# Optimization experiments

Measured on AMD Instinct MI355X. Metric: run time of the kernel, lower is better.

The kernel has to match this reference:

```python
import jax, jax.numpy as jnp
import numpy as np

B, N, C, KV = 4, 4096, 1024, 1024
H = 4            # hardcoded 4-way split in the source
Ch, Kh = C // H, KV // H
EPS = 1e-5       # InstanceNorm2d default eps


def setup_inputs() -> dict:
    key = jax.random.key(0)
    ks = jax.random.split(key, 12)
    s = 0.02
    return {
        "emb1":     jax.random.normal(ks[0], (B, N, C),  jnp.float32),
        "emb_all":  jax.random.normal(ks[1], (B, N, KV), jnp.float32),
        "embd1":    jax.random.normal(ks[2], (B, N, C),  jnp.float32),
        "emb_alld": jax.random.normal(ks[3], (B, N, KV), jnp.float32),
        # per-head query weights (distinct per split), torch Linear layout [out,in]
        "Wq":   jax.random.normal(ks[4],  (H, Ch, Ch), jnp.float32) * s,
        "Wqd":  jax.random.normal(ks[5],  (H, Ch, Ch), jnp.float32) * s,
        # source reuses key[0]/value[0] for all splits -> single shared weight
        "Wk0":  jax.random.normal(ks[6],  (Kh, Kh), jnp.float32) * s,
        "Wv0":  jax.random.normal(ks[7],  (Kh, Kh), jnp.float32) * s,
        "Wkd0": jax.random.normal(ks[8],  (Kh, Kh), jnp.float32) * s,
        "Wvd0": jax.random.normal(ks[9],  (Kh, Kh), jnp.float32) * s,
        "Wout":  jax.random.normal(ks[10], (C, C), jnp.float32) * s,
        "Woutd": jax.random.normal(ks[11], (C, C), jnp.float32) * s,
    }


def _inorm(s):
    # InstanceNorm2d(affine=False): normalize over the (C/4, KV/4) plane per (b, head)
    m = s.mean(axis=(2, 3), keepdims=True)
    v = ((s - m) ** 2).mean(axis=(2, 3), keepdims=True)
    return (s - m) * jax.lax.rsqrt(v + EPS)


def reference(emb1, emb_all, embd1, emb_alld,
              Wq, Wqd, Wk0, Wv0, Wkd0, Wvd0, Wout, Woutd):
    scale = 1.0 / np.sqrt(KV).astype(np.float32)
    # split into 4 channel groups and project (Q: per-group weight; K/V: shared weight)
    Q  = jnp.einsum('bnhc,hoc->bhno', emb1.reshape(B, N, H, Ch),  Wq)    # [B,H,N,Ch]
    Qd = jnp.einsum('bnhc,hoc->bhno', embd1.reshape(B, N, H, Ch), Wqd)
    K  = jnp.einsum('bnhk,ok->bhno', emb_all.reshape(B, N, H, Kh),  Wk0)  # [B,H,N,Kh]
    V  = jnp.einsum('bnhk,ok->bhno', emb_all.reshape(B, N, H, Kh),  Wv0)
    Kd = jnp.einsum('bnhk,ok->bhno', emb_alld.reshape(B, N, H, Kh), Wkd0)
    Vd = jnp.einsum('bnhk,ok->bhno', emb_alld.reshape(B, N, H, Kh), Wvd0)
    # channel-attention scores: contract over tokens N -> [B,H,Ch,Kh]
    s1  = jnp.einsum('bhnc,bhnk->bhck', Q,  Kd) * scale
    sd1 = jnp.einsum('bhnc,bhnk->bhck', Qd, K)  * scale
    p1  = jax.nn.softmax(_inorm(s1),  axis=-1)
    pd1 = jax.nn.softmax(_inorm(sd1), axis=-1)
    # context: probs @ V^T -> [b,h,c,n]; permute(0,3,2,1)+view -> [B,N,C] (c-major, h-minor)
    ctx1  = jnp.einsum('bhck,bhnk->bnch', p1,  Vd).reshape(B, N, C)
    ctxd1 = jnp.einsum('bhck,bhnk->bnch', pd1, V ).reshape(B, N, C)
    O1  = ctx1  @ Wout.T
    Od1 = ctxd1 @ Woutd.T
    return (O1, Od1)
```

## Files before the change

kernel.cpp:

```cpp
#include <hip/hip_runtime.h>
#include <math.h>


#define PITCH 40

typedef __bf16 bf16x4 __attribute__((ext_vector_type(4)));
typedef __bf16 bf16x8 __attribute__((ext_vector_type(8)));
typedef float f32x4 __attribute__((ext_vector_type(4)));

__device__ inline void gl2lds16(const void* g, void* l) {
    __builtin_amdgcn_global_load_lds(
        (const __attribute__((address_space(1))) unsigned int*)g,
        (__attribute__((address_space(3))) unsigned int*)l, 16, 0, 0);
}

__global__ __launch_bounds__(256) void prep_x(const float* __restrict__ emb_all,
                                              const float* __restrict__ emb_alld,
                                              __bf16* __restrict__ Xb) {
    const float* src = blockIdx.y ? emb_alld : emb_all;
    __bf16* dst = Xb + (long long)blockIdx.y * 16777216;
    long long i4 = (long long)blockIdx.x * 256 + threadIdx.x;
    float4 v = *(const float4*)&src[i4 * 4];
    bf16x4 o = {(__bf16)v.x, (__bf16)v.y, (__bf16)v.z, (__bf16)v.w};
    *(bf16x4*)&dst[i4 * 4] = o;
}

__global__ __launch_bounds__(256) void prep_w(
    const float* __restrict__ Wq, const float* __restrict__ Wqd,
    const float* __restrict__ Wk0, const float* __restrict__ Wv0,
    const float* __restrict__ Wkd0, const float* __restrict__ Wvd0,
    const float* __restrict__ Wout, const float* __restrict__ Woutd,
    __bf16* __restrict__ Wq_bf, __bf16* __restrict__ Wk_bf,
    __bf16* __restrict__ WvT_bf, __bf16* __restrict__ WoutR_bf)
{
    int id = blockIdx.x * 256 + threadIdx.x;
    if (id < 524288) {
        Wq_bf[id] = (__bf16)(id < 262144 ? Wq[id] : Wqd[id - 262144]);
    } else if (id < 655360) {
        int j = id - 524288;
        Wk_bf[j] = (__bf16)(j < 65536 ? Wkd0[j] : Wk0[j - 65536]);
    } else if (id < 786432) {
        int j = id - 655360;
        int p = j >> 16, r = (j >> 8) & 255, c2 = j & 255;
        const float* s = p ? Wv0 : Wvd0;
        WvT_bf[j] = (__bf16)s[c2 * 256 + r];
    } else if (id < 2883584) {
        int j = id - 786432;
        int p = j >> 20; int rem = j & 1048575; int h = rem >> 18; int oc = rem & 262143;
        int o = oc >> 8, c = oc & 255;
        const float* s = p ? Woutd : Wout;
        WoutR_bf[j] = (__bf16)s[o * 1024 + c * 4 + h];
    }
}

__global__ __launch_bounds__(256, 2) void gram_mfma(
    const float* __restrict__ emb1, const float* __restrict__ emb_all,
    const float* __restrict__ embd1, const float* __restrict__ emb_alld,
    float* __restrict__ Gpart)
{
    __shared__ __bf16 As[2][128 * PITCH];
    __shared__ __bf16 Bs[2][128 * PITCH];

    const int z = blockIdx.z;
    const int path = z >> 4, bh = z & 15;
    const int b = bh >> 2, h = bh & 3;
    const float* Xm = (path == 0 ? emb_alld : emb_all) + (long long)b * 4194304 + h * 256;
    const float* Xn = (path == 0 ? emb1     : embd1)   + (long long)b * 4194304 + h * 256;

    const int i0 = (blockIdx.x >> 1) * 128;
    const int j0 = (blockIdx.x & 1) * 128;
    const int kb0 = blockIdx.y * 1024;

    const int t = threadIdx.x;
    const int q  = t & 7;
    const int i4 = t >> 3;
    const int lane = t & 63;
    const int wave = t >> 6;
    const int wr = (wave >> 1) * 64, wc = (wave & 1) * 64;
    const int fm = lane & 15, fg = lane >> 4;

    f32x4 acc[4][4];
#pragma unroll
    for (int u = 0; u < 4; ++u)
#pragma unroll
        for (int v = 0; v < 4; ++v) acc[u][v] = (f32x4){0.f, 0.f, 0.f, 0.f};

    const float* pa = Xm + (long long)(kb0 + q * 4) * 1024 + i0 + i4 * 4;
    const float* pb = Xn + (long long)(kb0 + q * 4) * 1024 + j0 + i4 * 4;

    float4 vaA[4], vbA[4], vaB[4], vbB[4];
#pragma unroll
    for (int r = 0; r < 4; ++r) {
        vaA[r] = *(const float4*)(pa + (long long)r * 1024);
        vbA[r] = *(const float4*)(pb + (long long)r * 1024);
    }

#define GRAM_STEP(CURA, CURB, NXTA, NXTB, BUF, SOFF, GUARD)                         \
    do {                                                                            \
        if (GUARD) {                                                                \
            const float* qa = pa + (long long)(SOFF) * 32768;                       \
            const float* qb = pb + (long long)(SOFF) * 32768;                       \
            _Pragma("unroll")                                                       \
            for (int r = 0; r < 4; ++r) {                                           \
                NXTA[r] = *(const float4*)(qa + (long long)r * 1024);               \
                NXTB[r] = *(const float4*)(qb + (long long)r * 1024);               \
            }                                                                       \
        }                                                                           \
        _Pragma("unroll")                                                           \
        for (int cc = 0; cc < 4; ++cc) {                                            \
            bf16x4 wa, wb;                                                          \
            _Pragma("unroll")                                                       \
            for (int r = 0; r < 4; ++r) {                                           \
                wa[r] = (__bf16)(((const float*)&CURA[r])[cc]);                     \
                wb[r] = (__bf16)(((const float*)&CURB[r])[cc]);                     \
            }                                                                       \
            *(bf16x4*)&As[BUF][(i4 * 4 + cc) * PITCH + q * 4] = wa;                 \
            *(bf16x4*)&Bs[BUF][(i4 * 4 + cc) * PITCH + q * 4] = wb;                 \
        }                                                                           \
        asm volatile("s_waitcnt lgkmcnt(0)\ns_barrier" ::: "memory");               \
        bf16x8 af[4], bfv[4];                                                       \
        _Pragma("unroll")                                                           \
        for (int mt = 0; mt < 4; ++mt)                                              \
            af[mt] = *(const bf16x8*)&As[BUF][(wr + mt * 16 + fm) * PITCH + fg * 8];\
        _Pragma("unroll")                                                           \
        for (int nt = 0; nt < 4; ++nt)                                              \
            bfv[nt] = *(const bf16x8*)&Bs[BUF][(wc + nt * 16 + fm) * PITCH + fg * 8];\
        _Pragma("unroll")                                                           \
        for (int mt = 0; mt < 4; ++mt)                                              \
            _Pragma("unroll")                                                       \
            for (int nt = 0; nt < 4; ++nt)                                          \
                acc[mt][nt] = __builtin_amdgcn_mfma_f32_16x16x32_bf16(              \
                    af[mt], bfv[nt], acc[mt][nt], 0, 0, 0);                         \
    } while (0)

    for (int s = 0; s < 32; s += 2) {
        GRAM_STEP(vaA, vbA, vaB, vbB, 0, s + 1, true);
        GRAM_STEP(vaB, vbB, vaA, vbA, 1, s + 2, (s < 30));
    }
#undef GRAM_STEP

    float* Gp = Gpart + ((long long)blockIdx.y * 32 + z) * 65536;
    const int col = lane & 15, rq = (lane >> 4) * 4;
#pragma unroll
    for (int mt = 0; mt < 4; ++mt)
#pragma unroll
        for (int nt = 0; nt < 4; ++nt)
#pragma unroll
            for (int r = 0; r < 4; ++r)
                Gp[(i0 + wr + mt * 16 + rq + r) * 256 + (j0 + wc + nt * 16 + col)] = acc[mt][nt][r];
}

__global__ __launch_bounds__(256) void reduce_g(const float* __restrict__ Gpart, __bf16* __restrict__ GT) {
    long long idx4 = (long long)blockIdx.x * 256 + threadIdx.x;
    float4 a = *(const float4*)&Gpart[idx4 * 4];
    float4 b = *(const float4*)&Gpart[2097152 + idx4 * 4];
    float4 c = *(const float4*)&Gpart[4194304 + idx4 * 4];
    float4 d = *(const float4*)&Gpart[6291456 + idx4 * 4];
    bf16x4 o;
    o[0] = (__bf16)(a.x + b.x + c.x + d.x);
    o[1] = (__bf16)(a.y + b.y + c.y + d.y);
    o[2] = (__bf16)(a.z + b.z + c.z + d.z);
    o[3] = (__bf16)(a.w + b.w + c.w + d.w);
    *(bf16x4*)&GT[idx4 * 4] = o;
}

template <typename CT>
__global__ __launch_bounds__(256) void mfma_nt(
    const __bf16* __restrict__ A, const __bf16* __restrict__ B, CT* __restrict__ C,
    int mtiles, int K,
    long long a1, long long a2, long long a3,
    long long b1, long long b2, long long b3,
    long long c1, long long c2, long long c3,
    int cpitch, float alpha)
{
    __shared__ __bf16 As[64 * 32];
    __shared__ __bf16 Bs[64 * 32];
    const int z = blockIdx.y;
    const __bf16* Az = A + (long long)(z >> 4) * a1 + (long long)((z >> 2) & 3) * a2 + (long long)(z & 3) * a3;
    const __bf16* Bz = B + (long long)(z >> 4) * b1 + (long long)((z >> 2) & 3) * b2 + (long long)(z & 3) * b3;
    CT* Cz = C + (long long)(z >> 4) * c1 + (long long)((z >> 2) & 3) * c2 + (long long)(z & 3) * c3;

    const int tm = blockIdx.x % mtiles, tn = blockIdx.x / mtiles;
    const int t = threadIdx.x;
    const int lane = t & 63, wave = t >> 6;
    const int row = t >> 2, ch = t & 3;
    const int fm = lane & 15, fg = lane >> 4;

    const __bf16* ga = Az + (long long)(tm * 64 + row) * K + ch * 8;
    const __bf16* gb = Bz + (long long)(tn * 64 + row) * K + ch * 8;
    __bf16* la = &As[t * 8];
    __bf16* lb = &Bs[t * 8];

    f32x4 acc[4];
#pragma unroll
    for (int u = 0; u < 4; ++u) acc[u] = (f32x4){0.f, 0.f, 0.f, 0.f};

    for (int kb = 0; kb < K; kb += 32) {
        __syncthreads();
        gl2lds16(ga + kb, la);
        gl2lds16(gb + kb, lb);
        __syncthreads();
        bf16x8 bv = *(const bf16x8*)&Bs[(wave * 16 + fm) * 32 + fg * 8];
#pragma unroll
        for (int mt = 0; mt < 4; ++mt) {
            bf16x8 av = *(const bf16x8*)&As[(mt * 16 + fm) * 32 + fg * 8];
            acc[mt] = __builtin_amdgcn_mfma_f32_16x16x32_bf16(av, bv, acc[mt], 0, 0, 0);
        }
    }

    const int colc = tn * 64 + wave * 16 + fm;
    const int rq = fg * 4;
#pragma unroll
    for (int mt = 0; mt < 4; ++mt)
#pragma unroll
        for (int r = 0; r < 4; ++r) {
            int rowc = tm * 64 + mt * 16 + rq + r;
            Cz[(long long)rowc * cpitch + colc] = (CT)(acc[mt][r] * alpha);
        }
}


#define VMCNT8 asm volatile("s_waitcnt vmcnt(8)" ::: "memory")
#define VMCNT0 asm volatile("s_waitcnt vmcnt(0)" ::: "memory")
#define BARR   asm volatile("s_barrier" ::: "memory")

#define STAGE_A(h, kt, c) do { \
    _Pragma("unroll") \
    for (int o = 0; o < 2; ++o) { \
        int rl = (h) * 64 + o * 128 + stg_row; \
        gl2lds16(Xa + (long long)rl * 1024 + (kt) * 64 + stg_col, \
                 &lds[(c) * 32768 + rl * 64 + lin_col]); \
    } \
} while (0)

#define STAGE_B(h, kt, c) do { \
    _Pragma("unroll") \
    for (int o = 0; o < 2; ++o) { \
        int rl = o * 128 + (h) * 32 + (stg_row & 31) + ((stg_row & 32) << 1); \
        gl2lds16(Bb + (long long)rl * 1024 + (kt) * 64 + stg_col, \
                 &lds[(c) * 32768 + 16384 + rl * 64 + lin_col]); \
    } \
} while (0)

#define LOAD_A(hm, c) do { \
    _Pragma("unroll") \
    for (int mt = 0; mt < 4; ++mt) { \
        const __bf16* p = &lds[(c) * 32768 + (wr * 128 + (hm) * 64 + mt * 16 + fm) * 64]; \
        af[mt][0] = *(const bf16x8*)&p[(fg * 8) ^ rsw]; \
        af[mt][1] = *(const bf16x8*)&p[(32 + fg * 8) ^ rsw]; \
    } \
} while (0)

#define LOAD_B(hn, c) do { \
    _Pragma("unroll") \
    for (int nt = 0; nt < 2; ++nt) { \
        const __bf16* p = &lds[(c) * 32768 + 16384 + (wc * 64 + (hn) * 32 + nt * 16 + fm) * 64]; \
        bv[(hn) * 2 + nt][0] = *(const bf16x8*)&p[(fg * 8) ^ rsw]; \
        bv[(hn) * 2 + nt][1] = *(const bf16x8*)&p[(32 + fg * 8) ^ rsw]; \
    } \
} while (0)

#define MFMA_Q(hm, hn) do { \
    __builtin_amdgcn_s_setprio(1); \
    _Pragma("unroll") \
    for (int mt = 0; mt < 4; ++mt) \
        _Pragma("unroll") \
        for (int nt = 0; nt < 2; ++nt) { \
            acc[(hm) * 4 + mt][(hn) * 2 + nt] = __builtin_amdgcn_mfma_f32_16x16x32_bf16( \
                af[mt][0], bv[(hn) * 2 + nt][0], acc[(hm) * 4 + mt][(hn) * 2 + nt], 0, 0, 0); \
            acc[(hm) * 4 + mt][(hn) * 2 + nt] = __builtin_amdgcn_mfma_f32_16x16x32_bf16( \
                af[mt][1], bv[(hn) * 2 + nt][1], acc[(hm) * 4 + mt][(hn) * 2 + nt], 0, 0, 0); \
        } \
    __builtin_amdgcn_s_setprio(0); \
} while (0)

__global__ __launch_bounds__(512, 2) void obig8(
    const __bf16* __restrict__ Xall, const __bf16* __restrict__ Mb, float* __restrict__ out)
{
    __shared__ __bf16 lds[65536];

    const int id = blockIdx.x;
    const int wg = (id & 7) * 64 + (id >> 3);
    const int z = wg >> 6;
    const int tile = wg & 63;
    const int tm = tile & 15, tn = tile >> 4;
    const int path = z >> 2, b = z & 3;

    const __bf16* Xa = Xall + (path == 0 ? 16777216LL : 0LL)
                     + (long long)b * 4194304 + (long long)tm * 262144;
    const __bf16* Bb = Mb + (long long)path * 4194304 + (long long)b * 1048576
                     + (long long)tn * 262144;
    float* Ob = out + (long long)path * 16777216 + (long long)b * 4194304;

    const int t = threadIdx.x;
    const int lane = t & 63, wave = t >> 6;
    const int wr = wave >> 2, wc = wave & 3;
    const int fm = lane & 15, fg = lane >> 4;
    const int stg_row = t >> 3;
    const int lin_col = (t & 7) * 8;
    const int stg_col = ((t & 7) ^ (stg_row & 7)) * 8;
    const int rsw = (fm & 7) * 8;

    f32x4 acc[8][4];
#pragma unroll
    for (int u = 0; u < 8; ++u)
#pragma unroll
        for (int v = 0; v < 4; ++v) acc[u][v] = (f32x4){0.f, 0.f, 0.f, 0.f};

    bf16x8 af[4][2];
    bf16x8 bv[8][2];

    STAGE_A(0, 0, 0); STAGE_B(0, 0, 0); STAGE_B(1, 0, 0); STAGE_A(1, 0, 0);
    STAGE_A(0, 1, 1); STAGE_B(0, 1, 1); STAGE_B(1, 1, 1); STAGE_A(1, 1, 1);
    VMCNT8;
    BARR;

    for (int kt = 0; kt < 14; ++kt) {
        const int c = kt & 1;
        LOAD_A(0, c);
        LOAD_B(0, c);
        BARR;
        MFMA_Q(0, 0);
        BARR;
        LOAD_B(1, c);
        STAGE_A(0, kt + 2, c);
        BARR;
        MFMA_Q(0, 1);
        BARR;
        LOAD_A(1, c);
        STAGE_B(0, kt + 2, c);
        BARR;
        MFMA_Q(1, 1);
        BARR;
        STAGE_B(1, kt + 2, c);
        STAGE_A(1, kt + 2, c);
        VMCNT8;
        BARR;
        MFMA_Q(1, 0);
        BARR;
    }

    {
        LOAD_A(0, 0);
        LOAD_B(0, 0);
        BARR;
        MFMA_Q(0, 0);
        BARR;
        LOAD_B(1, 0);
        BARR;
        MFMA_Q(0, 1);
        BARR;
        LOAD_A(1, 0);
        BARR;
        MFMA_Q(1, 1);
        BARR;
        VMCNT0;
        BARR;
        MFMA_Q(1, 0);
        BARR;
    }

    {
        LOAD_A(0, 1);
        LOAD_B(0, 1);
        MFMA_Q(0, 0);
        LOAD_B(1, 1);
        MFMA_Q(0, 1);
        LOAD_A(1, 1);
        MFMA_Q(1, 1);
        MFMA_Q(1, 0);
    }

    const int rq = fg * 4;
    float* op = Ob + (long long)(tm * 256 + wr * 128 + rq) * 1024 + tn * 256 + wc * 64 + fm;
#pragma unroll
    for (int mi = 0; mi < 8; ++mi)
#pragma unroll
        for (int ni = 0; ni < 4; ++ni)
#pragma unroll
            for (int r = 0; r < 4; ++r)
                op[(long long)(mi * 16 + r) * 1024 + ni * 16] = acc[mi][ni][r];
}

__global__ __launch_bounds__(256) void stats1_kernel(const float* __restrict__ S,
                                                     float* __restrict__ pstat) {
    const int ch = blockIdx.x, pg = blockIdx.y;
    const float* s = S + (long long)pg * 65536 + ch * 8192;
    const int t = threadIdx.x;
    float sum = 0.f, sq = 0.f;
#pragma unroll
    for (int i = 0; i < 8; ++i) {
        float4 v = *(const float4*)&s[(i * 256 + t) * 4];
        sum += v.x + v.y + v.z + v.w;
        sq += v.x * v.x + v.y * v.y + v.z * v.z + v.w * v.w;
    }
#pragma unroll
    for (int off = 32; off; off >>= 1) {
        sum += __shfl_down(sum, off);
        sq  += __shfl_down(sq,  off);
    }
    __shared__ float r1[4], r2[4];
    int w = t >> 6;
    if ((t & 63) == 0) { r1[w] = sum; r2[w] = sq; }
    __syncthreads();
    if (t == 0) {
        pstat[(pg * 8 + ch) * 2 + 0] = r1[0] + r1[1] + r1[2] + r1[3];
        pstat[(pg * 8 + ch) * 2 + 1] = r2[0] + r2[1] + r2[2] + r2[3];
    }
}

__global__ __launch_bounds__(256) void softmax_kernel(const float* __restrict__ S,
                                                      const float* __restrict__ pstat,
                                                      __bf16* __restrict__ p_bf) {
    const int pg = blockIdx.y;
    float ts = 0.f, tq = 0.f;
#pragma unroll
    for (int i = 0; i < 8; ++i) {
        ts += pstat[(pg * 8 + i) * 2 + 0];
        tq += pstat[(pg * 8 + i) * 2 + 1];
    }
    const float mean = ts * (1.0f / 65536.0f);
    const float rstd = rsqrtf(tq * (1.0f / 65536.0f) - mean * mean + 1e-5f);

    const int wave = threadIdx.x >> 6, lane = threadIdx.x & 63;
    const int c = blockIdx.x * 4 + wave;
    const float* row = S + (long long)pg * 65536 + c * 256;
    float4 v = *(const float4*)&row[lane * 4];
    float x0 = (v.x - mean) * rstd, x1 = (v.y - mean) * rstd;
    float x2 = (v.z - mean) * rstd, x3 = (v.w - mean) * rstd;
    float m = fmaxf(fmaxf(x0, x1), fmaxf(x2, x3));
#pragma unroll
    for (int off = 32; off; off >>= 1) m = fmaxf(m, __shfl_xor(m, off));
    float e0 = expf(x0 - m), e1 = expf(x1 - m), e2 = expf(x2 - m), e3 = expf(x3 - m);
    float ssum = e0 + e1 + e2 + e3;
#pragma unroll
    for (int off = 32; off; off >>= 1) ssum += __shfl_xor(ssum, off);
    float inv = 1.0f / ssum;
    bf16x4 o = {(__bf16)(e0 * inv), (__bf16)(e1 * inv), (__bf16)(e2 * inv), (__bf16)(e3 * inv)};
    *(bf16x4*)&p_bf[(long long)pg * 65536 + c * 256 + lane * 4] = o;
}

extern "C" void kernel_launch(void* const* d_in, const int* in_sizes, int n_in,
                              void* d_out, int out_size, void* d_ws, size_t ws_size,
                              hipStream_t stream) {
    const float* emb1     = (const float*)d_in[0];
    const float* emb_all  = (const float*)d_in[1];
    const float* embd1    = (const float*)d_in[2];
    const float* emb_alld = (const float*)d_in[3];
    const float* Wq    = (const float*)d_in[4];
    const float* Wqd   = (const float*)d_in[5];
    const float* Wk0   = (const float*)d_in[6];
    const float* Wv0   = (const float*)d_in[7];
    const float* Wkd0  = (const float*)d_in[8];
    const float* Wvd0  = (const float*)d_in[9];
    const float* Wout  = (const float*)d_in[10];
    const float* Woutd = (const float*)d_in[11];
    float* out = (float*)d_out;

    float* ws = (float*)d_ws;
    float*  Gpart   = ws;
    __bf16* Mb_bf   = (__bf16*)ws;
    __bf16* X_bf    = (__bf16*)(ws + 8388608);
    __bf16* GT_bf   = (__bf16*)(ws + 25165824);
    __bf16* T_bf    = (__bf16*)(ws + 26214400);
    float*  S       = ws + 27262976;
    __bf16* p_bf    = (__bf16*)(ws + 29360128);
    __bf16* PT_bf   = (__bf16*)(ws + 30408704);
    __bf16* Wq_bf   = (__bf16*)(ws + 31457280);
    __bf16* Wk_bf   = (__bf16*)(ws + 31719424);
    __bf16* WvT_bf  = (__bf16*)(ws + 31784960);
    __bf16* WoutR_bf= (__bf16*)(ws + 31850496);
    float*  st      = ws + 32899072;

    dim3 blk(256);

    prep_x<<<dim3(16384, 2), blk, 0, stream>>>(emb_all, emb_alld, X_bf);
    prep_w<<<11264, blk, 0, stream>>>(Wq, Wqd, Wk0, Wv0, Wkd0, Wvd0, Wout, Woutd,
                                      Wq_bf, Wk_bf, WvT_bf, WoutR_bf);

    gram_mfma<<<dim3(4, 4, 32), blk, 0, stream>>>(emb1, emb_all, embd1, emb_alld, Gpart);
    reduce_g<<<2048, blk, 0, stream>>>(Gpart, GT_bf);

    mfma_nt<__bf16><<<dim3(16, 32), blk, 0, stream>>>(
        Wq_bf, GT_bf, T_bf, 4, 256,
        262144, 0, 65536,  1048576, 262144, 65536,  1048576, 262144, 65536, 256, 1.0f);
    mfma_nt<float><<<dim3(16, 32), blk, 0, stream>>>(
        T_bf, Wk_bf, S, 4, 256,
        1048576, 262144, 65536,  65536, 0, 0,  1048576, 262144, 65536, 256, 0.03125f);

    stats1_kernel<<<dim3(8, 32), blk, 0, stream>>>(S, st);
    softmax_kernel<<<dim3(64, 32), blk, 0, stream>>>(S, st, p_bf);

    mfma_nt<__bf16><<<dim3(16, 32), blk, 0, stream>>>(
        WvT_bf, p_bf, PT_bf, 4, 256,
        65536, 0, 0,  1048576, 262144, 65536,  1048576, 262144, 65536, 256, 1.0f);
    mfma_nt<__bf16><<<dim3(64, 32), blk, 0, stream>>>(
        WoutR_bf, PT_bf, Mb_bf, 16, 256,
        1048576, 0, 262144,  1048576, 262144, 65536,  4194304, 1048576, 256, 1024, 1.0f);

    obig8<<<dim3(512), dim3(512), 0, stream>>>(X_bf, Mb_bf, out);
}
```

Measured before the change: 507.5 us.

## Compute full 256x256 gram tile per block with 8-way token split

The gram kernel now uses 512-thread blocks, each computing the whole 256x256 per-head gram tile over 512 tokens. Before, four 128x128 blocks each covered 1024 tokens, so every fp32 input row was read twice from global memory; now each row is read once. In exchange, the number of partial sums doubles to eight, so reduce_g writes and reads twice as much partial data. The per-thread accumulator doubles to 128 floats, which risks register spills under the 512-thread launch bound. prep_x moves after the reduction because the larger partial buffer now overlaps the bf16 X workspace.

```diff
diff --git a/kernel.cpp b/kernel.cpp
--- a/kernel.cpp
+++ b/kernel.cpp
@@ -53,57 +53,56 @@
     }
 }
 
-__global__ __launch_bounds__(256, 2) void gram_mfma(
+__global__ __launch_bounds__(512, 2) void gram_mfma(
     const float* __restrict__ emb1, const float* __restrict__ emb_all,
     const float* __restrict__ embd1, const float* __restrict__ emb_alld,
     float* __restrict__ Gpart)
 {
-    __shared__ __bf16 As[2][128 * PITCH];
-    __shared__ __bf16 Bs[2][128 * PITCH];
-
-    const int z = blockIdx.z;
+    __shared__ __bf16 As[2][256 * PITCH];
+    __shared__ __bf16 Bs[2][256 * PITCH];
+
+    const int z = blockIdx.y;
+    const int split = blockIdx.x;
     const int path = z >> 4, bh = z & 15;
     const int b = bh >> 2, h = bh & 3;
     const float* Xm = (path == 0 ? emb_alld : emb_all) + (long long)b * 4194304 + h * 256;
     const float* Xn = (path == 0 ? emb1     : embd1)   + (long long)b * 4194304 + h * 256;
 
-    const int i0 = (blockIdx.x >> 1) * 128;
-    const int j0 = (blockIdx.x & 1) * 128;
-    const int kb0 = blockIdx.y * 1024;
+    const int kb0 = split * 512;
 
     const int t = threadIdx.x;
     const int q  = t & 7;
     const int i4 = t >> 3;
     const int lane = t & 63;
     const int wave = t >> 6;
-    const int wr = (wave >> 1) * 64, wc = (wave & 1) * 64;
+    const int wr = wave >> 2, wc = wave & 3;
     const int fm = lane & 15, fg = lane >> 4;
 
-    f32x4 acc[4][4];
-#pragma unroll
-    for (int u = 0; u < 4; ++u)
+    f32x4 acc[8][4];
+#pragma unroll
+    for (int u = 0; u < 8; ++u)
 #pragma unroll
         for (int v = 0; v < 4; ++v) acc[u][v] = (f32x4){0.f, 0.f, 0.f, 0.f};
 
-    const float* pa = Xm + (long long)(kb0 + q * 4) * 1024 + i0 + i4 * 4;
-    const float* pb = Xn + (long long)(kb0 + q * 4) * 1024 + j0 + i4 * 4;
-
-    float4 vaA[4], vbA[4], vaB[4], vbB[4];
+    const float* pa = Xm + (long long)(kb0 + q * 4) * 1024 + i4 * 4;
+    const float* pb = Xn + (long long)(kb0 + q * 4) * 1024 + i4 * 4;
+
+    float4 aA[4], bA[4], aB[4], bB[4];
 #pragma unroll
     for (int r = 0; r < 4; ++r) {
-        vaA[r] = *(const float4*)(pa + (long long)r * 1024);
-        vbA[r] = *(const float4*)(pb + (long long)r * 1024);
-    }
-
-#define GRAM_STEP(CURA, CURB, NXTA, NXTB, BUF, SOFF, GUARD)                         \
+        aA[r] = *(const float4*)(pa + (long long)r * 1024);
+        bA[r] = *(const float4*)(pb + (long long)r * 1024);
+    }
+
+#define GRAM_STEP(CA, CB, NA, NB, BUF, SOFF, GUARD)                                 \
     do {                                                                            \
         if (GUARD) {                                                                \
             const float* qa = pa + (long long)(SOFF) * 32768;                       \
             const float* qb = pb + (long long)(SOFF) * 32768;                       \
             _Pragma("unroll")                                                       \
             for (int r = 0; r < 4; ++r) {                                           \
-                NXTA[r] = *(const float4*)(qa + (long long)r * 1024);               \
-                NXTB[r] = *(const float4*)(qb + (long long)r * 1024);               \
+                NA[r] = *(const float4*)(qa + (long long)r * 1024);                 \
+                NB[r] = *(const float4*)(qb + (long long)r * 1024);                 \
             }                                                                       \
         }                                                                           \
         _Pragma("unroll")                                                           \
@@ -111,56 +110,59 @@
             bf16x4 wa, wb;                                                          \
             _Pragma("unroll")                                                       \
             for (int r = 0; r < 4; ++r) {                                           \
-                wa[r] = (__bf16)(((const float*)&CURA[r])[cc]);                     \
-                wb[r] = (__bf16)(((const float*)&CURB[r])[cc]);                     \
+                wa[r] = (__bf16)(((const float*)&CA[r])[cc]);                       \
+                wb[r] = (__bf16)(((const float*)&CB[r])[cc]);                       \
             }                                                                       \
             *(bf16x4*)&As[BUF][(i4 * 4 + cc) * PITCH + q * 4] = wa;                 \
             *(bf16x4*)&Bs[BUF][(i4 * 4 + cc) * PITCH + q * 4] = wb;                 \
         }                                                                           \
         asm volatile("s_waitcnt lgkmcnt(0)\ns_barrier" ::: "memory");               \
-        bf16x8 af[4], bfv[4];                                                       \
-        _Pragma("unroll")                                                           \
-        for (int mt = 0; mt < 4; ++mt)                                              \
-            af[mt] = *(const bf16x8*)&As[BUF][(wr + mt * 16 + fm) * PITCH + fg * 8];\
+        bf16x8 bfv[4];                                                              \
         _Pragma("unroll")                                                           \
         for (int nt = 0; nt < 4; ++nt)                                              \
-            bfv[nt] = *(const bf16x8*)&Bs[BUF][(wc + nt * 16 + fm) * PITCH + fg * 8];\
+            bfv[nt] = *(const bf16x8*)&Bs[BUF][(wc * 64 + nt * 16 + fm) * PITCH + fg * 8]; \
         _Pragma("unroll")                                                           \
-        for (int mt = 0; mt < 4; ++mt)                                              \
+        for (int mt = 0; mt < 8; ++mt) {                                            \
+            bf16x8 af = *(const bf16x8*)&As[BUF][(wr * 128 + mt * 16 + fm) * PITCH + fg * 8]; \
             _Pragma("unroll")                                                       \
             for (int nt = 0; nt < 4; ++nt)                                          \
                 acc[mt][nt] = __builtin_amdgcn_mfma_f32_16x16x32_bf16(              \
-                    af[mt], bfv[nt], acc[mt][nt], 0, 0, 0);                         \
+                    af, bfv[nt], acc[mt][nt], 0, 0, 0);                             \
+        }                                                                           \
     } while (0)
 
-    for (int s = 0; s < 32; s += 2) {
-        GRAM_STEP(vaA, vbA, vaB, vbB, 0, s + 1, true);
-        GRAM_STEP(vaB, vbB, vaA, vbA, 1, s + 2, (s < 30));
+    for (int s = 0; s < 16; s += 2) {
+        GRAM_STEP(aA, bA, aB, bB, 0, s + 1, true);
+        GRAM_STEP(aB, bB, aA, bA, 1, s + 2, (s < 14));
     }
 #undef GRAM_STEP
 
-    float* Gp = Gpart + ((long long)blockIdx.y * 32 + z) * 65536;
-    const int col = lane & 15, rq = (lane >> 4) * 4;
-#pragma unroll
-    for (int mt = 0; mt < 4; ++mt)
+    float* Gp = Gpart + ((long long)split * 32 + z) * 65536;
+    const int rq = fg * 4;
+#pragma unroll
+    for (int mt = 0; mt < 8; ++mt)
 #pragma unroll
         for (int nt = 0; nt < 4; ++nt)
 #pragma unroll
             for (int r = 0; r < 4; ++r)
-                Gp[(i0 + wr + mt * 16 + rq + r) * 256 + (j0 + wc + nt * 16 + col)] = acc[mt][nt][r];
+                Gp[(wr * 128 + mt * 16 + rq + r) * 256 + (wc * 64 + nt * 16 + fm)] = acc[mt][nt][r];
 }
 
 __global__ __launch_bounds__(256) void reduce_g(const float* __restrict__ Gpart, __bf16* __restrict__ GT) {
     long long idx4 = (long long)blockIdx.x * 256 + threadIdx.x;
-    float4 a = *(const float4*)&Gpart[idx4 * 4];
-    float4 b = *(const float4*)&Gpart[2097152 + idx4 * 4];
-    float4 c = *(const float4*)&Gpart[4194304 + idx4 * 4];
-    float4 d = *(const float4*)&Gpart[6291456 + idx4 * 4];
+    float4 s0 = *(const float4*)&Gpart[idx4 * 4];
+    float4 s1 = *(const float4*)&Gpart[2097152 + idx4 * 4];
+    float4 s2 = *(const float4*)&Gpart[4194304 + idx4 * 4];
+    float4 s3 = *(const float4*)&Gpart[6291456 + idx4 * 4];
+    float4 s4 = *(const float4*)&Gpart[8388608 + idx4 * 4];
+    float4 s5 = *(const float4*)&Gpart[10485760 + idx4 * 4];
+    float4 s6 = *(const float4*)&Gpart[12582912 + idx4 * 4];
+    float4 s7 = *(const float4*)&Gpart[14680064 + idx4 * 4];
     bf16x4 o;
-    o[0] = (__bf16)(a.x + b.x + c.x + d.x);
-    o[1] = (__bf16)(a.y + b.y + c.y + d.y);
-    o[2] = (__bf16)(a.z + b.z + c.z + d.z);
-    o[3] = (__bf16)(a.w + b.w + c.w + d.w);
+    o[0] = (__bf16)(((s0.x + s1.x) + (s2.x + s3.x)) + ((s4.x + s5.x) + (s6.x + s7.x)));
+    o[1] = (__bf16)(((s0.y + s1.y) + (s2.y + s3.y)) + ((s4.y + s5.y) + (s6.y + s7.y)));
+    o[2] = (__bf16)(((s0.z + s1.z) + (s2.z + s3.z)) + ((s4.z + s5.z) + (s6.z + s7.z)));
+    o[3] = (__bf16)(((s0.w + s1.w) + (s2.w + s3.w)) + ((s4.w + s5.w) + (s6.w + s7.w)));
     *(bf16x4*)&GT[idx4 * 4] = o;
 }
 
@@ -474,12 +476,13 @@
 
     dim3 blk(256);
 
-    prep_x<<<dim3(16384, 2), blk, 0, stream>>>(emb_all, emb_alld, X_bf);
     prep_w<<<11264, blk, 0, stream>>>(Wq, Wqd, Wk0, Wv0, Wkd0, Wvd0, Wout, Woutd,
                                       Wq_bf, Wk_bf, WvT_bf, WoutR_bf);
 
-    gram_mfma<<<dim3(4, 4, 32), blk, 0, stream>>>(emb1, emb_all, embd1, emb_alld, Gpart);
+    gram_mfma<<<dim3(8, 32), dim3(512), 0, stream>>>(emb1, emb_all, embd1, emb_alld, Gpart);
     reduce_g<<<2048, blk, 0, stream>>>(Gpart, GT_bf);
+
+    prep_x<<<dim3(16384, 2), blk, 0, stream>>>(emb_all, emb_alld, X_bf);
 
     mfma_nt<__bf16><<<dim3(16, 32), blk, 0, stream>>>(
         Wq_bf, GT_bf, T_bf, 4, 256,
```

After: 501.8 us. Within noise of the previous version (-1.1%).
